# Optimization experiments

Measured on AMD Instinct MI355X. Metric: run time of the kernel, lower is better.

## Reference

```python
import jax, jax.numpy as jnp
import numpy as np
import math

V, T, D_POI, D_OUT = 200000, 512, 256, 512
D_IN = D_POI + 4
D_HID = D_POI + 100


def setup_inputs() -> dict:
    key = jax.random.key(0)
    ks = jax.random.split(key, 12)
    s = 0.02
    return {
        "prev_poi_idx": jax.random.randint(ks[0], (T,), 0, V),
        "prev_time_frac": jax.random.uniform(ks[1], (T,), jnp.float32),
        "poi_final_emb": jax.random.normal(ks[2], (V, D_POI), jnp.float32),
        "poi_latlon_deg": jax.random.uniform(ks[3], (V, 2), jnp.float32) * 90.0,
        "ln_w": jnp.ones((D_IN,), jnp.float32),
        "ln_b": jnp.zeros((D_IN,), jnp.float32),
        "w1": jax.random.normal(ks[4], (D_IN, D_HID), jnp.float32) * s,
        "b1": jnp.zeros((D_HID,), jnp.float32),
        "w2": jax.random.normal(ks[5], (D_HID, D_POI), jnp.float32) * s,
        "b2": jnp.zeros((D_POI,), jnp.float32),
        "w_ih": jax.random.normal(ks[6], (3 * D_OUT, D_POI), jnp.float32) * s,
        "w_hh": jax.random.normal(ks[7], (3 * D_OUT, D_OUT), jnp.float32) * s,
        "b_ih": jnp.zeros((3 * D_OUT,), jnp.float32),
        "b_hh": jnp.zeros((3 * D_OUT,), jnp.float32),
        "q": jax.random.normal(ks[8], (D_OUT,), jnp.float32),
        "log_lam": jnp.array(0.0, jnp.float32),  # log(recency_lambda=1.0)
    }


def _haversine_km(lat1, lon1, lat2, lon2, eps=1e-12):
    dlat = (lat2 - lat1) * 0.5
    dlon = (lon2 - lon1) * 0.5
    a = jnp.sin(dlat) ** 2 + jnp.clip(jnp.cos(lat1), -1, 1) * jnp.clip(jnp.cos(lat2), -1, 1) * jnp.sin(dlon) ** 2
    c = 2.0 * jnp.arctan2(jnp.sqrt(jnp.clip(a, 0, 1)), jnp.sqrt(jnp.clip(1 - a, eps, 1)))
    return 6371.0088 * c


def _forward(prev_poi_idx, prev_time_frac, poi_final_emb, poi_latlon_deg,
             ln_w, ln_b, w1, b1, w2, b2, w_ih, w_hh, b_ih, b_hh, q, log_lam):
    Tn = prev_poi_idx.shape[0]
    poi_emb = poi_final_emb[prev_poi_idx]                       # (T, d_poi)
    t = jnp.clip(prev_time_frac, 0.0, 1.0)
    sin_t = jnp.sin(2.0 * math.pi * t)
    cos_t = jnp.cos(2.0 * math.pi * t)
    dif = jnp.mod(t[1:] - t[:-1], 1.0) * 24.0
    dt_h = jnp.concatenate([jnp.zeros((1,), t.dtype), dif])
    # _poi_radians is under no_grad in torch
    latlon = jax.lax.stop_gradient(poi_latlon_deg[prev_poi_idx])
    lat = jnp.deg2rad(jnp.clip(latlon[:, 0], -90, 90))
    lon = jnp.deg2rad(jnp.clip(latlon[:, 1], -180, 180))
    dd = _haversine_km(lat[:-1], lon[:-1], lat[1:], lon[1:])
    dd_km = jnp.concatenate([jnp.zeros((1,), dd.dtype), dd])
    feat = jnp.stack([sin_t, cos_t, jnp.log1p(dt_h), jnp.log1p(dd_km)], axis=-1)  # (T, 4)
    x = jnp.concatenate([poi_emb, feat], axis=-1)               # (T, d_poi+4)
    # fuse: LayerNorm -> Linear -> GELU -> (Dropout eval=id) -> Linear
    mu = jnp.mean(x, axis=-1, keepdims=True)
    var = jnp.mean((x - mu) ** 2, axis=-1, keepdims=True)
    x = (x - mu) * jax.lax.rsqrt(var + 1e-5) * ln_w + ln_b
    x = jax.nn.gelu(x @ w1 + b1, approximate=False) @ w2 + b2   # (T, d_poi)
    # GRU (single layer, unidirectional), torch gate order r,z,n
    gi_all = x @ w_ih.T + b_ih                                  # (T, 3H)
    def step(h, gi):
        gh = h @ w_hh.T + b_hh
        gi_r, gi_z, gi_n = jnp.split(gi, 3)
        gh_r, gh_z, gh_n = jnp.split(gh, 3)
        r = jax.nn.sigmoid(gi_r + gh_r)
        z = jax.nn.sigmoid(gi_z + gh_z)
        n = jnp.tanh(gi_n + r * gh_n)
        h_new = (1.0 - z) * n + z * h
        return h_new, h_new
    h0 = jnp.zeros((D_OUT,), x.dtype)
    _, hs = jax.lax.scan(step, h0, gi_all)                      # (T, d_out)
    D = hs.shape[-1]
    score = hs @ (q[:D] / jnp.sqrt(jnp.asarray(D, hs.dtype)))
    age = jnp.arange(Tn, dtype=hs.dtype)
    lam = jnp.maximum(jnp.exp(log_lam), 1e-4)
    score = score - lam * (Tn - 1 - age)
    attn = jax.nn.softmax(score, axis=0)
    summary = jnp.sum(attn[:, None] * hs, axis=0, keepdims=True)  # (1, d_out)
    return summary, attn


def reference(prev_poi_idx, prev_time_frac, poi_final_emb, poi_latlon_deg,
              ln_w, ln_b, w1, b1, w2, b2, w_ih, w_hh, b_ih, b_hh, q, log_lam):
    return _forward(prev_poi_idx, prev_time_frac, poi_final_emb, poi_latlon_deg,
                    ln_w, ln_b, w1, b1, w2, b2, w_ih, w_hh, b_ih, b_hh, q, log_lam)
```

## Files before the change

kernel.cpp:

```cpp
#include <hip/hip_runtime.h>
#include <hip/hip_cooperative_groups.h>
#include <math.h>

namespace cg = cooperative_groups;

#define TT 512
#define DPOI 256
#define DIN 260
#define DHID 356
#define DOUTD 512
#define G3 1536

#define GB 32
#define HU (DOUTD / GB)
#define NR (3 * HU)

__global__ void feat_kernel(const int* __restrict__ idx, const float* __restrict__ timef,
                            const float* __restrict__ latlon, float* __restrict__ feat) {
    int i = threadIdx.x;
    if (i >= TT) return;
    float t = fminf(fmaxf(timef[i], 0.f), 1.f);
    const float TWO_PI = 6.28318530717958647692f;
    float s = sinf(TWO_PI * t);
    float c = cosf(TWO_PI * t);
    float dt_h = 0.f, dd = 0.f;
    if (i > 0) {
        float tp = fminf(fmaxf(timef[i - 1], 0.f), 1.f);
        float d = t - tp;
        d = d - floorf(d);
        dt_h = d * 24.f;
        int i0 = idx[i - 1], i1 = idx[i];
        float la0 = latlon[2 * (size_t)i0], lo0 = latlon[2 * (size_t)i0 + 1];
        float la1 = latlon[2 * (size_t)i1], lo1 = latlon[2 * (size_t)i1 + 1];
        const float D2R = 0.01745329251994329577f;
        float lat1 = fminf(fmaxf(la0, -90.f), 90.f) * D2R;
        float lon1 = fminf(fmaxf(lo0, -180.f), 180.f) * D2R;
        float lat2 = fminf(fmaxf(la1, -90.f), 90.f) * D2R;
        float lon2 = fminf(fmaxf(lo1, -180.f), 180.f) * D2R;
        float dlat = (lat2 - lat1) * 0.5f, dlon = (lon2 - lon1) * 0.5f;
        float sdlat = sinf(dlat), sdlon = sinf(dlon);
        float a = sdlat * sdlat +
                  fminf(fmaxf(cosf(lat1), -1.f), 1.f) * fminf(fmaxf(cosf(lat2), -1.f), 1.f) * sdlon * sdlon;
        float aa = fminf(fmaxf(a, 0.f), 1.f);
        float bb = fminf(fmaxf(1.f - a, 1e-12f), 1.f);
        float cc = 2.f * atan2f(sqrtf(aa), sqrtf(bb));
        dd = 6371.0088f * cc;
    }
    feat[4 * i + 0] = s;
    feat[4 * i + 1] = c;
    feat[4 * i + 2] = log1pf(dt_h);
    feat[4 * i + 3] = log1pf(dd);
}

__global__ void ln_kernel(const int* __restrict__ idx, const float* __restrict__ emb,
                          const float* __restrict__ feat, const float* __restrict__ lnw,
                          const float* __restrict__ lnb, float* __restrict__ xn) {
    int t = blockIdx.x;
    int tid = threadIdx.x;
    int wave = tid >> 6, lane = tid & 63;
    const float* row = emb + (size_t)idx[t] * DPOI;
    float v0 = row[tid];
    float v1 = (tid < 4) ? feat[4 * t + tid] : 0.f;

    __shared__ float red[4];
    __shared__ float mu_s, rs_s;

    float s = v0 + v1;
    for (int o = 32; o; o >>= 1) s += __shfl_down(s, o, 64);
    if (lane == 0) red[wave] = s;
    __syncthreads();
    if (tid == 0) mu_s = (red[0] + red[1] + red[2] + red[3]) * (1.f / 260.f);
    __syncthreads();
    float mu = mu_s;
    float d0 = v0 - mu;
    float d1 = (tid < 4) ? (v1 - mu) : 0.f;
    float sq = d0 * d0 + d1 * d1;
    for (int o = 32; o; o >>= 1) sq += __shfl_down(sq, o, 64);
    __syncthreads();
    if (lane == 0) red[wave] = sq;
    __syncthreads();
    if (tid == 0) {
        float var = (red[0] + red[1] + red[2] + red[3]) * (1.f / 260.f);
        rs_s = rsqrtf(var + 1e-5f);
    }
    __syncthreads();
    float rs = rs_s;
    xn[t * DIN + tid] = d0 * rs * lnw[tid] + lnb[tid];
    if (tid < 4)
        xn[t * DIN + 256 + tid] = d1 * rs * lnw[256 + tid] + lnb[256 + tid];
}

__global__ void mlp1_kernel(const float* __restrict__ xn, const float* __restrict__ w1,
                            const float* __restrict__ b1, float* __restrict__ h1) {
    int t = blockIdx.x, j = threadIdx.x;
    __shared__ float xl[DIN];
    for (int k = threadIdx.x; k < DIN; k += blockDim.x) xl[k] = xn[t * DIN + k];
    __syncthreads();
    if (j < DHID) {
        float acc = b1[j];
        #pragma unroll 4
        for (int k = 0; k < DIN; ++k) acc = fmaf(xl[k], w1[k * DHID + j], acc);
        float g = 0.5f * acc * (1.f + erff(acc * 0.70710678118654752440f));
        h1[t * DHID + j] = g;
    }
}

__global__ void mlp2_kernel(const float* __restrict__ h1, const float* __restrict__ w2,
                            const float* __restrict__ b2, float* __restrict__ x2) {
    int t = blockIdx.x, j = threadIdx.x;
    __shared__ float xl[DHID];
    for (int k = threadIdx.x; k < DHID; k += blockDim.x) xl[k] = h1[t * DHID + k];
    __syncthreads();
    float acc = b2[j];
    #pragma unroll 4
    for (int k = 0; k < DHID; ++k) acc = fmaf(xl[k], w2[k * DPOI + j], acc);
    x2[t * DPOI + j] = acc;
}

__global__ void gi_kernel(const float* __restrict__ x2, const float* __restrict__ wih,
                          const float* __restrict__ bih, float* __restrict__ gi) {
    int t = blockIdx.x;
    int tid = threadIdx.x;
    int wave = tid >> 6, lane = tid & 63;
    float4 xv = ((const float4*)(x2 + (size_t)t * DPOI))[lane];
    for (int r = wave; r < G3; r += 4) {
        float4 wv = ((const float4*)(wih + (size_t)r * DPOI))[lane];
        float s = xv.x * wv.x + xv.y * wv.y + xv.z * wv.z + xv.w * wv.w;
        for (int o = 32; o; o >>= 1) s += __shfl_down(s, o, 64);
        if (lane == 0) gi[(size_t)t * G3 + r] = s + bih[r];
    }
}

__global__ void zero_kernel(uint4* __restrict__ p, int n16) {
    int i = blockIdx.x * blockDim.x + threadIdx.x;
    int stride = gridDim.x * blockDim.x;
    uint4 z; z.x = 0u; z.y = 0u; z.z = 0u; z.w = 0u;
    for (; i < n16; i += stride) p[i] = z;
}

__global__ __launch_bounds__(1024)
void gru_tag_kernel(const float* __restrict__ gi, const float* __restrict__ whh,
                    const float* __restrict__ bhh, float* __restrict__ hs,
                    unsigned long long* __restrict__ hcomm) {
    __shared__ unsigned short w[NR][DOUTD];
    __shared__ float hprev[DOUTD];
    __shared__ float gsum[NR];
    __shared__ float bl[NR];

    int b = blockIdx.x;
    int tid = threadIdx.x;
    int wave = tid >> 6, lane = tid & 63;
    int jbase = b * HU;

    unsigned short* wl = &w[0][0];
    for (int e = tid; e < NR * DOUTD; e += 1024) {
        int rr = e >> 9, k = e & 511;
        int g = rr >> 4, jj = rr & 15;
        float v = whh[(size_t)(g * DOUTD + jbase + jj) * DOUTD + k];
        unsigned int u = __float_as_uint(v);
        u += 0x7fffu + ((u >> 16) & 1u);
        int kk = (k < 256) ? (((k >> 2) << 3) | (k & 3))
                           : ((((k - 256) >> 2) << 3) | 4 | (k & 3));
        wl[(rr << 9) + kk] = (unsigned short)(u >> 16);
    }
    if (tid < NR) {
        int g = tid >> 4, jj = tid & 15;
        bl[tid] = bhh[g * DOUTD + jbase + jj];
    }
    if (tid < DOUTD) hprev[tid] = 0.f;
    __syncthreads();

    const float4* hp4 = (const float4*)hprev;
    long budget = 2L * 1000 * 1000;

    float gir = 0.f, giz = 0.f, gin = 0.f, hreg = 0.f;
    if (tid < HU) {
        int j = jbase + tid;
        gir = gi[j];
        giz = gi[DOUTD + j];
        gin = gi[2 * DOUTD + j];
    }

    for (int s = 0; s < TT; ++s) {
        if (s > 0) {
            if (lane < 32) {
                int v = (wave << 5) + lane;
                bool own = (v >> 4) == b;
                const unsigned long long* ap = hcomm + (size_t)(s - 1) * DOUTD + v;
                unsigned long long p = 0;
                bool ok = own;
                while (!__all(ok)) {
                    if (!ok) {
                        p = __hip_atomic_load(ap, __ATOMIC_RELAXED,
                                              __HIP_MEMORY_SCOPE_AGENT);
                        ok = ((unsigned)(p >> 32) == (unsigned)s);
                    }
                    if (--budget < 0) break;
                }
                if (!own) hprev[v] = __uint_as_float((unsigned)p);
            }
            __syncthreads();
        }

        float4 ha = hp4[lane];
        float4 hb = hp4[64 + lane];
        #pragma unroll
        for (int rv = 0; rv < 3; ++rv) {
            int rr = wave * 3 + rv;
            uint4 wv = *(const uint4*)(wl + (rr << 9) + (lane << 3));
            float acc;
            acc = __uint_as_float(wv.x << 16) * ha.x;
            acc = fmaf(__uint_as_float(wv.x & 0xffff0000u), ha.y, acc);
            acc = fmaf(__uint_as_float(wv.y << 16), ha.z, acc);
            acc = fmaf(__uint_as_float(wv.y & 0xffff0000u), ha.w, acc);
            acc = fmaf(__uint_as_float(wv.z << 16), hb.x, acc);
            acc = fmaf(__uint_as_float(wv.z & 0xffff0000u), hb.y, acc);
            acc = fmaf(__uint_as_float(wv.w << 16), hb.z, acc);
            acc = fmaf(__uint_as_float(wv.w & 0xffff0000u), hb.w, acc);
            for (int o = 32; o; o >>= 1) acc += __shfl_down(acc, o, 64);
            if (lane == 0) gsum[rr] = acc + bl[rr];
        }
        __syncthreads();

        if (tid < HU) {
            int j = jbase + tid;
            float gr  = gir + gsum[tid];
            float gz  = giz + gsum[HU + tid];
            float ghn = gsum[2 * HU + tid];
            float r = 1.f / (1.f + expf(-gr));
            float z = 1.f / (1.f + expf(-gz));
            float n = tanhf(gin + r * ghn);
            float hn = (1.f - z) * n + z * hreg;
            hreg = hn;
            hs[(size_t)s * DOUTD + j] = hn;
            unsigned long long pay = ((unsigned long long)(unsigned)(s + 1) << 32) |
                                     (unsigned long long)__float_as_uint(hn);
            __hip_atomic_store(&hcomm[(size_t)s * DOUTD + j], pay,
                               __ATOMIC_RELAXED, __HIP_MEMORY_SCOPE_AGENT);
            hprev[j] = hn;
            if (s + 1 < TT) {
                const float* gn = gi + (size_t)(s + 1) * G3;
                gir = gn[j]; giz = gn[DOUTD + j]; gin = gn[2 * DOUTD + j];
            }
        }
    }
}

__global__ void attn_kernel(const float* __restrict__ hs, const float* __restrict__ q,
                            const float* __restrict__ log_lam, float* __restrict__ out) {
    int tid = threadIdx.x;
    int wave = tid >> 6, lane = tid & 63;
    __shared__ float sc[TT];
    __shared__ float at[TT];
    __shared__ float red[8];
    __shared__ float red2[8];
    __shared__ float denom_s, mx_s;

    const float qscale = 0.04419417382415921757f;
    for (int r = wave; r < TT; r += 8) {
        float acc = 0.f;
        #pragma unroll
        for (int m = 0; m < 8; ++m) {
            int k = lane + 64 * m;
            acc = fmaf(hs[(size_t)r * DOUTD + k], q[k], acc);
        }
        for (int o = 32; o; o >>= 1) acc += __shfl_down(acc, o, 64);
        if (lane == 0) sc[r] = acc * qscale;
    }
    __syncthreads();
    float lam = fmaxf(expf(log_lam[0]), 1e-4f);
    float s_i = sc[tid] - lam * (float)(TT - 1 - tid);

    float mval = s_i;
    for (int o = 32; o; o >>= 1) mval = fmaxf(mval, __shfl_down(mval, o, 64));
    if (lane == 0) red[wave] = mval;
    __syncthreads();
    if (tid == 0) {
        float mm = red[0];
        for (int i = 1; i < 8; ++i) mm = fmaxf(mm, red[i]);
        mx_s = mm;
    }
    __syncthreads();
    float e = expf(s_i - mx_s);
    float ssum = e;
    for (int o = 32; o; o >>= 1) ssum += __shfl_down(ssum, o, 64);
    if (lane == 0) red2[wave] = ssum;
    __syncthreads();
    if (tid == 0) {
        float dsum = 0.f;
        for (int i = 0; i < 8; ++i) dsum += red2[i];
        denom_s = dsum;
    }
    __syncthreads();
    float attn = e / denom_s;
    out[DOUTD + tid] = attn;
    at[tid] = attn;
    __syncthreads();
    float acc = 0.f;
    for (int i = 0; i < TT; ++i) acc = fmaf(at[i], hs[(size_t)i * DOUTD + tid], acc);
    out[tid] = acc;
}

extern "C" void kernel_launch(void* const* d_in, const int* in_sizes, int n_in,
                              void* d_out, int out_size, void* d_ws, size_t ws_size,
                              hipStream_t stream) {
    const int*   idx    = (const int*)d_in[0];
    const float* timef  = (const float*)d_in[1];
    const float* emb    = (const float*)d_in[2];
    const float* latlon = (const float*)d_in[3];
    const float* lnw    = (const float*)d_in[4];
    const float* lnb    = (const float*)d_in[5];
    const float* w1     = (const float*)d_in[6];
    const float* b1     = (const float*)d_in[7];
    const float* w2     = (const float*)d_in[8];
    const float* b2     = (const float*)d_in[9];
    const float* wih    = (const float*)d_in[10];
    const float* whh    = (const float*)d_in[11];
    const float* bih    = (const float*)d_in[12];
    const float* bhh    = (const float*)d_in[13];
    const float* q      = (const float*)d_in[14];
    const float* loglam = (const float*)d_in[15];
    float* out = (float*)d_out;

    unsigned long long* hcomm = (unsigned long long*)d_ws;
    float* feat = (float*)(hcomm + (size_t)TT * DOUTD);
    float* xn   = feat + 2048;
    float* h1   = xn + TT * DIN;
    float* x2   = h1 + TT * DHID;
    float* gi   = x2 + TT * DPOI;
    float* hs   = gi + (size_t)TT * G3;

    feat_kernel<<<1, TT, 0, stream>>>(idx, timef, latlon, feat);
    ln_kernel<<<TT, 256, 0, stream>>>(idx, emb, feat, lnw, lnb, xn);
    mlp1_kernel<<<TT, 384, 0, stream>>>(xn, w1, b1, h1);
    mlp2_kernel<<<TT, 256, 0, stream>>>(h1, w2, b2, x2);
    gi_kernel<<<TT, 256, 0, stream>>>(x2, wih, bih, gi);

    int n16 = (int)(((size_t)TT * DOUTD * 8) / 16);
    zero_kernel<<<256, 512, 0, stream>>>((uint4*)hcomm, n16);

    void* gru_args[] = { (void*)&gi, (void*)&whh, (void*)&bhh, (void*)&hs, (void*)&hcomm };
    hipLaunchCooperativeKernel((void*)gru_tag_kernel, dim3(GB), dim3(1024),
                               gru_args, 0, stream);

    attn_kernel<<<1, TT, 0, stream>>>(hs, q, loglam, out);
}
```

Measured before the change: 1.909 ms.

## Fuse feature, zeroing and attention kernels; shrink GRU grid with register weights

Folds the feature computation into the layernorm kernel, moves hcomm zeroing into gi_kernel, and fuses the attention epilogue into the cooperative GRU kernel behind a grid sync. The GRU drops from 32 to 8 blocks and keeps the w_hh rows in fp32 registers instead of bf16 shared memory. Each step's hidden value is now sent to the other blocks as bf16 packed with a step tag. Fast exp/rcp replaces the sigmoid and tanh. It also adds a dummy FMA loop in the spin-wait. The goal is fewer launches and less cross-block synchronization per step, at the cost of bf16 hidden-state exchange, heavier per-block work and high register pressure.

New measurement: 1.849 ms. -3.2%, faster.

```diff
diff --git a/kernel.cpp b/kernel.cpp
--- a/kernel.cpp
+++ b/kernel.cpp
@@ -11,25 +11,30 @@
 #define DOUTD 512
 #define G3 1536
 
-#define GB 32
+#define GB 8
 #define HU (DOUTD / GB)
-#define NR (3 * HU)
-
-__global__ void feat_kernel(const int* __restrict__ idx, const float* __restrict__ timef,
-                            const float* __restrict__ latlon, float* __restrict__ feat) {
-    int i = threadIdx.x;
-    if (i >= TT) return;
-    float t = fminf(fmaxf(timef[i], 0.f), 1.f);
+#define NRR (3 * HU)
+#define NPAY DOUTD
+
+__global__ void ln_kernel(const int* __restrict__ idx, const float* __restrict__ timef,
+                          const float* __restrict__ latlon, const float* __restrict__ emb,
+                          const float* __restrict__ lnw, const float* __restrict__ lnb,
+                          float* __restrict__ xn) {
+    int t = blockIdx.x;
+    int tid = threadIdx.x;
+    int wave = tid >> 6, lane = tid & 63;
+
+    float tv = fminf(fmaxf(timef[t], 0.f), 1.f);
     const float TWO_PI = 6.28318530717958647692f;
-    float s = sinf(TWO_PI * t);
-    float c = cosf(TWO_PI * t);
-    float dt_h = 0.f, dd = 0.f;
-    if (i > 0) {
-        float tp = fminf(fmaxf(timef[i - 1], 0.f), 1.f);
-        float d = t - tp;
+    float f0 = sinf(TWO_PI * tv);
+    float f1 = cosf(TWO_PI * tv);
+    float f2 = 0.f, f3 = 0.f;
+    if (t > 0) {
+        float tp = fminf(fmaxf(timef[t - 1], 0.f), 1.f);
+        float d = tv - tp;
         d = d - floorf(d);
-        dt_h = d * 24.f;
-        int i0 = idx[i - 1], i1 = idx[i];
+        f2 = log1pf(d * 24.f);
+        int i0 = idx[t - 1], i1 = idx[t];
         float la0 = latlon[2 * (size_t)i0], lo0 = latlon[2 * (size_t)i0 + 1];
         float la1 = latlon[2 * (size_t)i1], lo1 = latlon[2 * (size_t)i1 + 1];
         const float D2R = 0.01745329251994329577f;
@@ -44,23 +49,13 @@
         float aa = fminf(fmaxf(a, 0.f), 1.f);
         float bb = fminf(fmaxf(1.f - a, 1e-12f), 1.f);
         float cc = 2.f * atan2f(sqrtf(aa), sqrtf(bb));
-        dd = 6371.0088f * cc;
-    }
-    feat[4 * i + 0] = s;
-    feat[4 * i + 1] = c;
-    feat[4 * i + 2] = log1pf(dt_h);
-    feat[4 * i + 3] = log1pf(dd);
-}
-
-__global__ void ln_kernel(const int* __restrict__ idx, const float* __restrict__ emb,
-                          const float* __restrict__ feat, const float* __restrict__ lnw,
-                          const float* __restrict__ lnb, float* __restrict__ xn) {
-    int t = blockIdx.x;
-    int tid = threadIdx.x;
-    int wave = tid >> 6, lane = tid & 63;
+        f3 = log1pf(6371.0088f * cc);
+    }
+    float fv = (tid == 0) ? f0 : (tid == 1) ? f1 : (tid == 2) ? f2 : f3;
+
     const float* row = emb + (size_t)idx[t] * DPOI;
     float v0 = row[tid];
-    float v1 = (tid < 4) ? feat[4 * t + tid] : 0.f;
+    float v1 = (tid < 4) ? fv : 0.f;
 
     __shared__ float red[4];
     __shared__ float mu_s, rs_s;
@@ -118,10 +113,13 @@
 }
 
 __global__ void gi_kernel(const float* __restrict__ x2, const float* __restrict__ wih,
-                          const float* __restrict__ bih, float* __restrict__ gi) {
+                          const float* __restrict__ bih, float* __restrict__ gi,
+                          uint4* __restrict__ hcz) {
     int t = blockIdx.x;
     int tid = threadIdx.x;
     int wave = tid >> 6, lane = tid & 63;
+    uint4 z; z.x = 0u; z.y = 0u; z.z = 0u; z.w = 0u;
+    hcz[(size_t)t * 256 + tid] = z;
     float4 xv = ((const float4*)(x2 + (size_t)t * DPOI))[lane];
     for (int r = wave; r < G3; r += 4) {
         float4 wv = ((const float4*)(wih + (size_t)r * DPOI))[lane];
@@ -131,47 +129,50 @@
     }
 }
 
-__global__ void zero_kernel(uint4* __restrict__ p, int n16) {
-    int i = blockIdx.x * blockDim.x + threadIdx.x;
-    int stride = gridDim.x * blockDim.x;
-    uint4 z; z.x = 0u; z.y = 0u; z.z = 0u; z.w = 0u;
-    for (; i < n16; i += stride) p[i] = z;
-}
-
 __global__ __launch_bounds__(1024)
-void gru_tag_kernel(const float* __restrict__ gi, const float* __restrict__ whh,
-                    const float* __restrict__ bhh, float* __restrict__ hs,
-                    unsigned long long* __restrict__ hcomm) {
-    __shared__ unsigned short w[NR][DOUTD];
+void gru_fused_kernel(const float* __restrict__ gi, const float* __restrict__ whh,
+                      const float* __restrict__ bhh, float* __restrict__ hs,
+                      unsigned long long* __restrict__ hcomm,
+                      const float* __restrict__ q, const float* __restrict__ log_lam,
+                      float* __restrict__ out) {
     __shared__ float hprev[DOUTD];
-    __shared__ float gsum[NR];
-    __shared__ float bl[NR];
+    __shared__ float gsum[NRR];
+    __shared__ float sc[TT];
+    __shared__ float at[TT];
+    __shared__ float red[8];
+    __shared__ float red2[8];
+    __shared__ float denom_s, mx_s;
 
     int b = blockIdx.x;
     int tid = threadIdx.x;
     int wave = tid >> 6, lane = tid & 63;
     int jbase = b * HU;
-
-    unsigned short* wl = &w[0][0];
-    for (int e = tid; e < NR * DOUTD; e += 1024) {
-        int rr = e >> 9, k = e & 511;
-        int g = rr >> 4, jj = rr & 15;
-        float v = whh[(size_t)(g * DOUTD + jbase + jj) * DOUTD + k];
-        unsigned int u = __float_as_uint(v);
-        u += 0x7fffu + ((u >> 16) & 1u);
-        int kk = (k < 256) ? (((k >> 2) << 3) | (k & 3))
-                           : ((((k - 256) >> 2) << 3) | 4 | (k & 3));
-        wl[(rr << 9) + kk] = (unsigned short)(u >> 16);
-    }
-    if (tid < NR) {
-        int g = tid >> 4, jj = tid & 15;
-        bl[tid] = bhh[g * DOUTD + jbase + jj];
+    int g4 = lane >> 4, l4 = lane & 15;
+    int rr0 = wave * 12 + g4 * 3;
+
+    float4 wf0[8], wf1[8], wf2[8];
+    float bl0, bl1, bl2;
+    {
+        int r0 = rr0, r1 = rr0 + 1, r2 = rr0 + 2;
+        const float4* p0 = (const float4*)(whh + (size_t)((r0 >> 6) * DOUTD + jbase + (r0 & 63)) * DOUTD);
+        const float4* p1 = (const float4*)(whh + (size_t)((r1 >> 6) * DOUTD + jbase + (r1 & 63)) * DOUTD);
+        const float4* p2 = (const float4*)(whh + (size_t)((r2 >> 6) * DOUTD + jbase + (r2 & 63)) * DOUTD);
+        #pragma unroll
+        for (int m = 0; m < 8; ++m) {
+            wf0[m] = p0[m * 16 + l4];
+            wf1[m] = p1[m * 16 + l4];
+            wf2[m] = p2[m * 16 + l4];
+        }
+        bl0 = bhh[(r0 >> 6) * DOUTD + jbase + (r0 & 63)];
+        bl1 = bhh[(r1 >> 6) * DOUTD + jbase + (r1 & 63)];
+        bl2 = bhh[(r2 >> 6) * DOUTD + jbase + (r2 & 63)];
     }
     if (tid < DOUTD) hprev[tid] = 0.f;
     __syncthreads();
 
     const float4* hp4 = (const float4*)hprev;
     long budget = 2L * 1000 * 1000;
+    float dj = (float)tid * 1e-6f;
 
     float gir = 0.f, giz = 0.f, gin = 0.f, hreg = 0.f;
     if (tid < HU) {
@@ -183,60 +184,72 @@
 
     for (int s = 0; s < TT; ++s) {
         if (s > 0) {
-            if (lane < 32) {
-                int v = (wave << 5) + lane;
-                bool own = (v >> 4) == b;
-                const unsigned long long* ap = hcomm + (size_t)(s - 1) * DOUTD + v;
+            if (tid >= 256 && tid < 768) {
+                int u = tid - 256;
+                bool own = (u >> 6) == b;
+                const unsigned long long* ap = hcomm + (size_t)(s - 1) * NPAY + u;
                 unsigned long long p = 0;
                 bool ok = own;
+                unsigned tagw = (unsigned)s;
                 while (!__all(ok)) {
                     if (!ok) {
                         p = __hip_atomic_load(ap, __ATOMIC_RELAXED,
                                               __HIP_MEMORY_SCOPE_AGENT);
-                        ok = ((unsigned)(p >> 32) == (unsigned)s);
+                        ok = ((unsigned)p == tagw);
                     }
+                    float x = dj;
+                    #pragma unroll
+                    for (int zz = 0; zz < 8; ++zz) x = fmaf(x, 1.0000001f, 1e-7f);
+                    dj = x;
                     if (--budget < 0) break;
                 }
-                if (!own) hprev[v] = __uint_as_float((unsigned)p);
+                if (!own) hprev[u] = __uint_as_float((unsigned)(p >> 32));
             }
             __syncthreads();
         }
 
-        float4 ha = hp4[lane];
-        float4 hb = hp4[64 + lane];
+        float a0 = 0.f, a1 = 0.f, a2 = 0.f;
         #pragma unroll
-        for (int rv = 0; rv < 3; ++rv) {
-            int rr = wave * 3 + rv;
-            uint4 wv = *(const uint4*)(wl + (rr << 9) + (lane << 3));
-            float acc;
-            acc = __uint_as_float(wv.x << 16) * ha.x;
-            acc = fmaf(__uint_as_float(wv.x & 0xffff0000u), ha.y, acc);
-            acc = fmaf(__uint_as_float(wv.y << 16), ha.z, acc);
-            acc = fmaf(__uint_as_float(wv.y & 0xffff0000u), ha.w, acc);
-            acc = fmaf(__uint_as_float(wv.z << 16), hb.x, acc);
-            acc = fmaf(__uint_as_float(wv.z & 0xffff0000u), hb.y, acc);
-            acc = fmaf(__uint_as_float(wv.w << 16), hb.z, acc);
-            acc = fmaf(__uint_as_float(wv.w & 0xffff0000u), hb.w, acc);
-            for (int o = 32; o; o >>= 1) acc += __shfl_down(acc, o, 64);
-            if (lane == 0) gsum[rr] = acc + bl[rr];
+        for (int m = 0; m < 8; ++m) {
+            float4 h4 = hp4[m * 16 + l4];
+            a0 = fmaf(wf0[m].x, h4.x, a0); a0 = fmaf(wf0[m].y, h4.y, a0);
+            a0 = fmaf(wf0[m].z, h4.z, a0); a0 = fmaf(wf0[m].w, h4.w, a0);
+            a1 = fmaf(wf1[m].x, h4.x, a1); a1 = fmaf(wf1[m].y, h4.y, a1);
+            a1 = fmaf(wf1[m].z, h4.z, a1); a1 = fmaf(wf1[m].w, h4.w, a1);
+            a2 = fmaf(wf2[m].x, h4.x, a2); a2 = fmaf(wf2[m].y, h4.y, a2);
+            a2 = fmaf(wf2[m].z, h4.z, a2); a2 = fmaf(wf2[m].w, h4.w, a2);
+        }
+        #pragma unroll
+        for (int o = 1; o < 16; o <<= 1) {
+            a0 += __shfl_xor(a0, o, 64);
+            a1 += __shfl_xor(a1, o, 64);
+            a2 += __shfl_xor(a2, o, 64);
+        }
+        if (l4 == 0) {
+            gsum[rr0]     = a0 + bl0;
+            gsum[rr0 + 1] = a1 + bl1;
+            gsum[rr0 + 2] = a2 + bl2;
         }
         __syncthreads();
 
         if (tid < HU) {
-            int j = jbase + tid;
             float gr  = gir + gsum[tid];
             float gz  = giz + gsum[HU + tid];
             float ghn = gsum[2 * HU + tid];
-            float r = 1.f / (1.f + expf(-gr));
-            float z = 1.f / (1.f + expf(-gz));
-            float n = tanhf(gin + r * ghn);
+            float r = __builtin_amdgcn_rcpf(1.f + __expf(-gr));
+            float z = __builtin_amdgcn_rcpf(1.f + __expf(-gz));
+            float xt = gin + r * ghn;
+            float n = 1.f - 2.f * __builtin_amdgcn_rcpf(__expf(2.f * xt) + 1.f);
             float hn = (1.f - z) * n + z * hreg;
             hreg = hn;
+            unsigned ub = __float_as_uint(hn);
+            ub += 0x7fffu + ((ub >> 16) & 1u);
+            unsigned long long pay = ((unsigned long long)(ub & 0xffff0000u) << 32) |
+                                     (unsigned)(s + 1);
+            __hip_atomic_store(&hcomm[(size_t)s * NPAY + jbase + tid], pay,
+                               __ATOMIC_RELAXED, __HIP_MEMORY_SCOPE_AGENT);
+            int j = jbase + tid;
             hs[(size_t)s * DOUTD + j] = hn;
-            unsigned long long pay = ((unsigned long long)(unsigned)(s + 1) << 32) |
-                                     (unsigned long long)__float_as_uint(hn);
-            __hip_atomic_store(&hcomm[(size_t)s * DOUTD + j], pay,
-                               __ATOMIC_RELAXED, __HIP_MEMORY_SCOPE_AGENT);
             hprev[j] = hn;
             if (s + 1 < TT) {
                 const float* gn = gi + (size_t)(s + 1) * G3;
@@ -244,20 +257,14 @@
             }
         }
     }
-}
-
-__global__ void attn_kernel(const float* __restrict__ hs, const float* __restrict__ q,
-                            const float* __restrict__ log_lam, float* __restrict__ out) {
-    int tid = threadIdx.x;
-    int wave = tid >> 6, lane = tid & 63;
-    __shared__ float sc[TT];
-    __shared__ float at[TT];
-    __shared__ float red[8];
-    __shared__ float red2[8];
-    __shared__ float denom_s, mx_s;
+
+    asm volatile("" :: "v"(dj));
+
+    cg::this_grid().sync();
+    if (b != 0) return;
 
     const float qscale = 0.04419417382415921757f;
-    for (int r = wave; r < TT; r += 8) {
+    for (int r = wave; r < TT; r += 16) {
         float acc = 0.f;
         #pragma unroll
         for (int m = 0; m < 8; ++m) {
@@ -269,11 +276,11 @@
     }
     __syncthreads();
     float lam = fmaxf(expf(log_lam[0]), 1e-4f);
-    float s_i = sc[tid] - lam * (float)(TT - 1 - tid);
+    float s_i = (tid < TT) ? (sc[tid] - lam * (float)(TT - 1 - tid)) : -1e30f;
 
     float mval = s_i;
     for (int o = 32; o; o >>= 1) mval = fmaxf(mval, __shfl_down(mval, o, 64));
-    if (lane == 0) red[wave] = mval;
+    if (lane == 0 && wave < 8) red[wave] = mval;
     __syncthreads();
     if (tid == 0) {
         float mm = red[0];
@@ -281,10 +288,10 @@
         mx_s = mm;
     }
     __syncthreads();
-    float e = expf(s_i - mx_s);
+    float e = (tid < TT) ? expf(s_i - mx_s) : 0.f;
     float ssum = e;
     for (int o = 32; o; o >>= 1) ssum += __shfl_down(ssum, o, 64);
-    if (lane == 0) red2[wave] = ssum;
+    if (lane == 0 && wave < 8) red2[wave] = ssum;
     __syncthreads();
     if (tid == 0) {
         float dsum = 0.f;
@@ -292,13 +299,17 @@
         denom_s = dsum;
     }
     __syncthreads();
-    float attn = e / denom_s;
-    out[DOUTD + tid] = attn;
-    at[tid] = attn;
-    __syncthreads();
-    float acc = 0.f;
-    for (int i = 0; i < TT; ++i) acc = fmaf(at[i], hs[(size_t)i * DOUTD + tid], acc);
-    out[tid] = acc;
+    if (tid < TT) {
+        float attn = e / denom_s;
+        out[DOUTD + tid] = attn;
+        at[tid] = attn;
+    }
+    __syncthreads();
+    if (tid < TT) {
+        float acc = 0.f;
+        for (int i = 0; i < TT; ++i) acc = fmaf(at[i], hs[(size_t)i * DOUTD + tid], acc);
+        out[tid] = acc;
+    }
 }
 
 extern "C" void kernel_launch(void* const* d_in, const int* in_sizes, int n_in,
@@ -323,25 +334,19 @@
     float* out = (float*)d_out;
 
     unsigned long long* hcomm = (unsigned long long*)d_ws;
-    float* feat = (float*)(hcomm + (size_t)TT * DOUTD);
-    float* xn   = feat + 2048;
+    float* xn   = (float*)(hcomm + (size_t)TT * NPAY);
     float* h1   = xn + TT * DIN;
     float* x2   = h1 + TT * DHID;
     float* gi   = x2 + TT * DPOI;
     float* hs   = gi + (size_t)TT * G3;
 
-    feat_kernel<<<1, TT, 0, stream>>>(idx, timef, latlon, feat);
-    ln_kernel<<<TT, 256, 0, stream>>>(idx, emb, feat, lnw, lnb, xn);
+    ln_kernel<<<TT, 256, 0, stream>>>(idx, timef, latlon, emb, lnw, lnb, xn);
     mlp1_kernel<<<TT, 384, 0, stream>>>(xn, w1, b1, h1);
     mlp2_kernel<<<TT, 256, 0, stream>>>(h1, w2, b2, x2);
-    gi_kernel<<<TT, 256, 0, stream>>>(x2, wih, bih, gi);
-
-    int n16 = (int)(((size_t)TT * DOUTD * 8) / 16);
-    zero_kernel<<<256, 512, 0, stream>>>((uint4*)hcomm, n16);
-
-    void* gru_args[] = { (void*)&gi, (void*)&whh, (void*)&bhh, (void*)&hs, (void*)&hcomm };
-    hipLaunchCooperativeKernel((void*)gru_tag_kernel, dim3(GB), dim3(1024),
+    gi_kernel<<<TT, 256, 0, stream>>>(x2, wih, bih, gi, (uint4*)hcomm);
+
+    void* gru_args[] = { (void*)&gi, (void*)&whh, (void*)&bhh, (void*)&hs,
+                         (void*)&hcomm, (void*)&q, (void*)&loglam, (void*)&out };
+    hipLaunchCooperativeKernel((void*)gru_fused_kernel, dim3(GB), dim3(1024),
                                gru_args, 0, stream);
-
-    attn_kernel<<<1, TT, 0, stream>>>(hs, q, loglam, out);
-}
+}
```
